# Performance work log

Hardware: AMD Instinct MI355X
Metric: run time of the kernel (lower is better)

## Reference

```python
import jax, jax.numpy as jnp
import numpy as np

NIN, NOUT = 256, 64

def setup_inputs() -> dict:
    key = jax.random.key(0)
    k1, k2, k3, k4 = jax.random.split(key, 4)
    B, T = 4, 4096
    y = jax.random.normal(k1, (B, T, NIN), dtype=jnp.float32)
    # torch Linear(nin, nout).weight has shape [nout, nin]; store as [nin, nout]
    s = 1.0 / np.sqrt(NIN)
    Wq = jax.random.uniform(k2, (NIN, NOUT), jnp.float32, -s, s)
    Wk = jax.random.uniform(k3, (NIN, NOUT), jnp.float32, -s, s)
    Wv = jax.random.uniform(k4, (NIN, NOUT), jnp.float32, -s, s)
    return {"y": y, "Wq": Wq, "Wk": Wk, "Wv": Wv}

def reference(y, Wq, Wk, Wv):
    T = y.shape[1]
    que = y @ Wq  # [B,T,NOUT]
    key = y @ Wk
    val = y @ Wv
    att = jnp.einsum('bqd,bkd->bqk', que, key)  # [B,T,T]
    causal = jnp.tril(jnp.ones((T, T), dtype=bool))  # True = keep
    att = jnp.where(causal, att, -jnp.inf)
    att = jax.nn.softmax(att / jnp.sqrt(jnp.float32(NOUT)), axis=-1)
    return jnp.einsum('bqk,bkd->bqd', att, val)
```

## Files before the change

### kernel.cpp

```cpp
#include <hip/hip_runtime.h>
#include <hip/hip_bf16.h>

#define TLEN 4096
#define NINP 256
#define DD   64

#define QSCALE 0.18033688011112042f

typedef __attribute__((ext_vector_type(8))) short bf16x8;
typedef __attribute__((ext_vector_type(4))) float f32x4;

union U8 { bf16x8 v; uint u[4]; };
union F32U { float f; uint u; };

__device__ inline ushort bfu(float x) {
    F32U a; a.f = x;
    uint r = a.u + 0x7fffu + ((a.u >> 16) & 1u);
    return (ushort)(r >> 16);
}
__device__ inline uint pk2(float p0, float p1) {
    F32U a, b; a.f = p0; b.f = p1;
    return __builtin_amdgcn_perm(b.u + 0x8000u, a.u + 0x8000u, 0x07060302u);
}
__device__ inline bf16x8 ld16(const ushort* p) {
    return *(const bf16x8*)p;
}
__device__ inline bf16x8 ld8x2(const ushort* p) {
    U8 u;
    uint2 a = *(const uint2*)p;
    uint2 b = *(const uint2*)(p + 4);
    u.u[0] = a.x; u.u[1] = a.y; u.u[2] = b.x; u.u[3] = b.y;
    return u.v;
}

__global__ __launch_bounds__(256) void prep_wt(
    const float* __restrict__ Wq, const float* __restrict__ Wk,
    const float* __restrict__ Wv, ushort* __restrict__ WT)
{
    const int t = threadIdx.x;
    const int m = blockIdx.x >> 4;
    const int d0 = (blockIdx.x & 15) * 4;
    const float* W = (m == 0) ? Wq : ((m == 1) ? Wk : Wv);
    const float scale = (m == 0) ? QSCALE : 1.0f;
    float4 v = *(const float4*)&W[t * DD + d0];
    WT[m * 16384 + (d0 + 0) * 256 + t] = bfu(v.x * scale);
    WT[m * 16384 + (d0 + 1) * 256 + t] = bfu(v.y * scale);
    WT[m * 16384 + (d0 + 2) * 256 + t] = bfu(v.z * scale);
    WT[m * 16384 + (d0 + 3) * 256 + t] = bfu(v.w * scale);
}

__global__ __launch_bounds__(256, 2) void qkv_kernel(
    const float* __restrict__ y, const ushort* __restrict__ WT,
    ushort* __restrict__ Qh, ushort* __restrict__ Kh, ushort* __restrict__ VhT)
{
    __shared__ ushort Wl[64 * 260];
    __shared__ ushort tb[2304];

    const int t = threadIdx.x;
    const int w = t >> 6, lane = t & 63;
    const int quad = lane >> 4, l15 = lane & 15;
    const int rgrp = w & 1, ngrp = w >> 1;
    const int rowbase = blockIdx.x * 32;
    const int myrow = rowbase + rgrp * 16 + l15;

    bf16x8 afrag[8];
    const float* yrow = y + (size_t)myrow * NINP;
    #pragma unroll
    for (int s = 0; s < 8; ++s) {
        float4 lo = *(const float4*)&yrow[s * 32 + quad * 8];
        float4 hi = *(const float4*)&yrow[s * 32 + quad * 8 + 4];
        U8 u;
        u.u[0] = bfu(lo.x) | (uint(bfu(lo.y)) << 16);
        u.u[1] = bfu(lo.z) | (uint(bfu(lo.w)) << 16);
        u.u[2] = bfu(hi.x) | (uint(bfu(hi.y)) << 16);
        u.u[3] = bfu(hi.z) | (uint(bfu(hi.w)) << 16);
        afrag[s] = u.v;
    }

    f32x4 acc[3][2];
    #pragma unroll
    for (int m = 0; m < 3; ++m)
        #pragma unroll
        for (int nj = 0; nj < 2; ++nj)
            acc[m][nj] = f32x4{0.f, 0.f, 0.f, 0.f};

    for (int m = 0; m < 3; ++m) {
        __syncthreads();
        {
            int n = t >> 2, seg = t & 3;
            const ushort* src = WT + m * 16384 + n * 256 + seg * 64;
            ushort* dst = &Wl[n * 260 + seg * 64];
            #pragma unroll
            for (int j = 0; j < 16; ++j)
                ((uint2*)dst)[j] = ((const uint2*)src)[j];
        }
        __syncthreads();
        #pragma unroll
        for (int s = 0; s < 8; ++s)
            #pragma unroll
            for (int nj = 0; nj < 2; ++nj) {
                int nt = ngrp * 2 + nj;
                bf16x8 bfrag = ld8x2(&Wl[(nt * 16 + l15) * 260 + s * 32 + quad * 8]);
                acc[m][nj] = __builtin_amdgcn_mfma_f32_16x16x32_bf16(
                    afrag[s], bfrag, acc[m][nj], 0, 0, 0);
            }
    }

    for (int m = 0; m < 2; ++m) {
        __syncthreads();
        #pragma unroll
        for (int nj = 0; nj < 2; ++nj) {
            int nt = ngrp * 2 + nj;
            #pragma unroll
            for (int r = 0; r < 4; ++r)
                tb[(rgrp * 16 + quad * 4 + r) * 68 + nt * 16 + l15] = bfu(acc[m][nj][r]);
        }
        __syncthreads();
        int row = t >> 3, c0 = (t & 7) * 8;
        ushort* gd = (m == 0 ? Qh : Kh) + (size_t)(rowbase + row) * DD + c0;
        const ushort* sp = &tb[row * 68 + c0];
        ((uint2*)gd)[0] = ((const uint2*)sp)[0];
        ((uint2*)gd)[1] = ((const uint2*)sp)[1];
    }

    __syncthreads();
    #pragma unroll
    for (int nj = 0; nj < 2; ++nj) {
        int nt = ngrp * 2 + nj;
        int d = nt * 16 + l15;
        #pragma unroll
        for (int r = 0; r < 4; r += 2) {
            int tt = rgrp * 16 + quad * 4 + r;
            *(uint*)&tb[d * 36 + tt] = pk2(acc[2][nj][r], acc[2][nj][r + 1]);
        }
    }
    __syncthreads();
    {
        int d = t >> 2, seg = t & 3;
        int bb = blockIdx.x >> 7;
        int tofs = (blockIdx.x & 127) * 32 + seg * 8;
        ushort* gv = VhT + ((size_t)bb * DD + d) * TLEN + tofs;
        const ushort* sp = &tb[d * 36 + seg * 8];
        ((uint2*)gv)[0] = ((const uint2*)sp)[0];
        ((uint2*)gv)[1] = ((const uint2*)sp)[1];
    }
}

template <bool MASK>
__device__ inline void softmax_store(
    f32x4 st[2][4], ushort* Pw, int qb, int c0, int l15, int quad, float* l_acc)
{
    #pragma unroll
    for (int qt = 0; qt < 2; ++qt) {
        const int q = qb + qt * 16 + l15;
        #pragma unroll
        for (int kt = 0; kt < 4; ++kt) {
            const int kbase = c0 + kt * 16 + quad * 4;
            float p[4];
            #pragma unroll
            for (int r = 0; r < 4; ++r) {
                float e = exp2f(st[qt][kt][r]);
                p[r] = (!MASK || (kbase + r <= q)) ? e : 0.f;
                l_acc[qt] += p[r];
            }
            ushort* pw = Pw + (qt * 16 + l15) * 68 + kt * 16 + quad * 4;
            *(uint*)&pw[0] = pk2(p[0], p[1]);
            *(uint*)&pw[2] = pk2(p[2], p[3]);
        }
    }
}

__global__ __launch_bounds__(512, 2) void attn_kernel(
    const ushort* __restrict__ Qh, const ushort* __restrict__ Kh,
    const ushort* __restrict__ VhT, float* __restrict__ out)
{
    __shared__ ushort Pb[8][32 * 68];
    __shared__ float  Ob[8][2048];
    __shared__ float  lb[8][32];

    const int t = threadIdx.x;
    const int w = t >> 6, lane = t & 63;
    const int quad = lane >> 4, l15 = lane & 15;
    const int b = blockIdx.x >> 6;
    const int pr = blockIdx.x & 63;

    const ushort* Qb = Qh + (size_t)b * TLEN * DD;
    const ushort* Kb = Kh + (size_t)b * TLEN * DD;
    const ushort* Vb = VhT + (size_t)b * DD * TLEN;
    float* outb = out + (size_t)b * TLEN * DD;

    for (int half = 0; half < 2; ++half) {
        const int tile = (half == 0) ? pr : (127 - pr);
        const int seg  = (half == 0) ? w : (7 - w);
        const int qb   = tile * 32;
        const int nc   = (tile + 2) >> 1;
        const int cps  = (nc + 7) >> 3;
        const int clo  = seg * cps;
        const int chi  = (nc < clo + cps) ? nc : (clo + cps);

        f32x4 o_acc[2][4];
        #pragma unroll
        for (int qt = 0; qt < 2; ++qt)
            #pragma unroll
            for (int nt = 0; nt < 4; ++nt)
                o_acc[qt][nt] = f32x4{0.f, 0.f, 0.f, 0.f};
        float l_acc[2] = {0.f, 0.f};

        if (clo < chi) {
            bf16x8 qf[2][2];
            #pragma unroll
            for (int qt = 0; qt < 2; ++qt)
                #pragma unroll
                for (int s = 0; s < 2; ++s)
                    qf[qt][s] = ld16(Qb + (size_t)(qb + qt * 16 + l15) * DD + s * 32 + quad * 8);

            bf16x8 kf[4][2];
            {
                int c0 = clo * 64;
                #pragma unroll
                for (int kt = 0; kt < 4; ++kt)
                    #pragma unroll
                    for (int s = 0; s < 2; ++s)
                        kf[kt][s] = ld16(Kb + (size_t)(c0 + kt * 16 + l15) * DD + s * 32 + quad * 8);
            }

            for (int ci = clo; ci < chi; ++ci) {
                const int c0 = ci * 64;
                bf16x8 vf[4][2];
                #pragma unroll
                for (int nt = 0; nt < 4; ++nt)
                    #pragma unroll
                    for (int s = 0; s < 2; ++s)
                        vf[nt][s] = ld16(Vb + (size_t)(nt * 16 + l15) * TLEN + c0 + s * 32 + quad * 8);

                f32x4 st[2][4];
                #pragma unroll
                for (int qt = 0; qt < 2; ++qt)
                    #pragma unroll
                    for (int kt = 0; kt < 4; ++kt)
                        st[qt][kt] = f32x4{0.f, 0.f, 0.f, 0.f};
                #pragma unroll
                for (int s = 0; s < 2; ++s)
                    #pragma unroll
                    for (int qt = 0; qt < 2; ++qt)
                        #pragma unroll
                        for (int kt = 0; kt < 4; ++kt)
                            st[qt][kt] = __builtin_amdgcn_mfma_f32_16x16x32_bf16(
                                kf[kt][s], qf[qt][s], st[qt][kt], 0, 0, 0);

                if (ci + 1 < chi) {
                    int c1 = c0 + 64;
                    #pragma unroll
                    for (int kt = 0; kt < 4; ++kt)
                        #pragma unroll
                        for (int s = 0; s < 2; ++s)
                            kf[kt][s] = ld16(Kb + (size_t)(c1 + kt * 16 + l15) * DD + s * 32 + quad * 8);
                }

                if (ci == nc - 1)
                    softmax_store<true>(st, Pb[w], qb, c0, l15, quad, l_acc);
                else
                    softmax_store<false>(st, Pb[w], qb, c0, l15, quad, l_acc);

                #pragma unroll
                for (int qt = 0; qt < 2; ++qt) {
                    const ushort* pr_ = &Pb[w][(qt * 16 + l15) * 68];
                    bf16x8 ap0 = ld8x2(pr_ + quad * 8);
                    bf16x8 ap1 = ld8x2(pr_ + 32 + quad * 8);
                    #pragma unroll
                    for (int nt = 0; nt < 4; ++nt) {
                        o_acc[qt][nt] = __builtin_amdgcn_mfma_f32_16x16x32_bf16(
                            ap0, vf[nt][0], o_acc[qt][nt], 0, 0, 0);
                        o_acc[qt][nt] = __builtin_amdgcn_mfma_f32_16x16x32_bf16(
                            ap1, vf[nt][1], o_acc[qt][nt], 0, 0, 0);
                    }
                }
            }

            #pragma unroll
            for (int qt = 0; qt < 2; ++qt) {
                l_acc[qt] += __shfl_xor(l_acc[qt], 16, 64);
                l_acc[qt] += __shfl_xor(l_acc[qt], 32, 64);
            }
        }

        #pragma unroll
        for (int qt = 0; qt < 2; ++qt) {
            #pragma unroll
            for (int nt = 0; nt < 4; ++nt)
                #pragma unroll
                for (int r = 0; r < 4; ++r)
                    Ob[w][(qt * 16 + quad * 4 + r) * 64 + nt * 16 + l15] = o_acc[qt][nt][r];
            if (quad == 0) lb[w][qt * 16 + l15] = l_acc[qt];
        }
        __syncthreads();

        {
            int q = t >> 4, d0 = (t & 15) * 4;
            f32x4 s = f32x4{0.f, 0.f, 0.f, 0.f};
            float ls = 0.f;
            #pragma unroll
            for (int ww = 0; ww < 8; ++ww) {
                s += *(const f32x4*)&Ob[ww][q * 64 + d0];
                ls += lb[ww][q];
            }
            float inv = __builtin_amdgcn_rcpf(ls);
            float4 r;
            r.x = s[0] * inv; r.y = s[1] * inv; r.z = s[2] * inv; r.w = s[3] * inv;
            *(float4*)&outb[(size_t)(qb + q) * DD + d0] = r;
        }
        __syncthreads();
    }
}

extern "C" void kernel_launch(void* const* d_in, const int* in_sizes, int n_in,
                              void* d_out, int out_size, void* d_ws, size_t ws_size,
                              hipStream_t stream) {
    const float* y  = (const float*)d_in[0];
    const float* Wq = (const float*)d_in[1];
    const float* Wk = (const float*)d_in[2];
    const float* Wv = (const float*)d_in[3];
    float* outp = (float*)d_out;

    const int rows = in_sizes[0] / NINP;
    const int nb = rows / TLEN;

    ushort* WT  = (ushort*)d_ws;
    ushort* Qh  = WT + 3 * 16384;
    ushort* Kh  = Qh + (size_t)rows * DD;
    ushort* VhT = Kh + (size_t)rows * DD;

    prep_wt<<<48, 256, 0, stream>>>(Wq, Wk, Wv, WT);
    qkv_kernel<<<rows / 32, 256, 0, stream>>>(y, WT, Qh, Kh, VhT);
    attn_kernel<<<nb * 64, 512, 0, stream>>>(Qh, Kh, VhT, outp);
}
```

Baseline: 116.5 us.

## Fuse QKV projection and attention into one kernel with per-batch grid barrier

Merges the QKV projection and attention kernels into a single launch. Each block first projects 64 rows, then waits on a per-batch atomic counter before running attention. Blocks drop from 512 to 256 threads, so the key-chunk split per tile goes from 8 waves to 4, and shared memory is reused through a union. This removes one kernel launch and the gap between kernels, but it relies on all 256 blocks being co-resident for the spin barrier and halves the waves available for attention parallelism.

```diff
diff --git a/kernel.cpp b/kernel.cpp
--- a/kernel.cpp
+++ b/kernel.cpp
@@ -35,8 +35,9 @@
 
 __global__ __launch_bounds__(256) void prep_wt(
     const float* __restrict__ Wq, const float* __restrict__ Wk,
-    const float* __restrict__ Wv, ushort* __restrict__ WT)
+    const float* __restrict__ Wv, ushort* __restrict__ WT, uint* __restrict__ cnt)
 {
+    if (blockIdx.x == 0 && threadIdx.x < 8) cnt[threadIdx.x] = 0;
     const int t = threadIdx.x;
     const int m = blockIdx.x >> 4;
     const int d0 = (blockIdx.x & 15) * 4;
@@ -49,102 +50,10 @@
     WT[m * 16384 + (d0 + 3) * 256 + t] = bfu(v.w * scale);
 }
 
-__global__ __launch_bounds__(256, 2) void qkv_kernel(
-    const float* __restrict__ y, const ushort* __restrict__ WT,
-    ushort* __restrict__ Qh, ushort* __restrict__ Kh, ushort* __restrict__ VhT)
-{
-    __shared__ ushort Wl[64 * 260];
-    __shared__ ushort tb[2304];
-
-    const int t = threadIdx.x;
-    const int w = t >> 6, lane = t & 63;
-    const int quad = lane >> 4, l15 = lane & 15;
-    const int rgrp = w & 1, ngrp = w >> 1;
-    const int rowbase = blockIdx.x * 32;
-    const int myrow = rowbase + rgrp * 16 + l15;
-
-    bf16x8 afrag[8];
-    const float* yrow = y + (size_t)myrow * NINP;
-    #pragma unroll
-    for (int s = 0; s < 8; ++s) {
-        float4 lo = *(const float4*)&yrow[s * 32 + quad * 8];
-        float4 hi = *(const float4*)&yrow[s * 32 + quad * 8 + 4];
-        U8 u;
-        u.u[0] = bfu(lo.x) | (uint(bfu(lo.y)) << 16);
-        u.u[1] = bfu(lo.z) | (uint(bfu(lo.w)) << 16);
-        u.u[2] = bfu(hi.x) | (uint(bfu(hi.y)) << 16);
-        u.u[3] = bfu(hi.z) | (uint(bfu(hi.w)) << 16);
-        afrag[s] = u.v;
-    }
-
-    f32x4 acc[3][2];
-    #pragma unroll
-    for (int m = 0; m < 3; ++m)
-        #pragma unroll
-        for (int nj = 0; nj < 2; ++nj)
-            acc[m][nj] = f32x4{0.f, 0.f, 0.f, 0.f};
-
-    for (int m = 0; m < 3; ++m) {
-        __syncthreads();
-        {
-            int n = t >> 2, seg = t & 3;
-            const ushort* src = WT + m * 16384 + n * 256 + seg * 64;
-            ushort* dst = &Wl[n * 260 + seg * 64];
-            #pragma unroll
-            for (int j = 0; j < 16; ++j)
-                ((uint2*)dst)[j] = ((const uint2*)src)[j];
-        }
-        __syncthreads();
-        #pragma unroll
-        for (int s = 0; s < 8; ++s)
-            #pragma unroll
-            for (int nj = 0; nj < 2; ++nj) {
-                int nt = ngrp * 2 + nj;
-                bf16x8 bfrag = ld8x2(&Wl[(nt * 16 + l15) * 260 + s * 32 + quad * 8]);
-                acc[m][nj] = __builtin_amdgcn_mfma_f32_16x16x32_bf16(
-                    afrag[s], bfrag, acc[m][nj], 0, 0, 0);
-            }
-    }
-
-    for (int m = 0; m < 2; ++m) {
-        __syncthreads();
-        #pragma unroll
-        for (int nj = 0; nj < 2; ++nj) {
-            int nt = ngrp * 2 + nj;
-            #pragma unroll
-            for (int r = 0; r < 4; ++r)
-                tb[(rgrp * 16 + quad * 4 + r) * 68 + nt * 16 + l15] = bfu(acc[m][nj][r]);
-        }
-        __syncthreads();
-        int row = t >> 3, c0 = (t & 7) * 8;
-        ushort* gd = (m == 0 ? Qh : Kh) + (size_t)(rowbase + row) * DD + c0;
-        const ushort* sp = &tb[row * 68 + c0];
-        ((uint2*)gd)[0] = ((const uint2*)sp)[0];
-        ((uint2*)gd)[1] = ((const uint2*)sp)[1];
-    }
-
-    __syncthreads();
-    #pragma unroll
-    for (int nj = 0; nj < 2; ++nj) {
-        int nt = ngrp * 2 + nj;
-        int d = nt * 16 + l15;
-        #pragma unroll
-        for (int r = 0; r < 4; r += 2) {
-            int tt = rgrp * 16 + quad * 4 + r;
-            *(uint*)&tb[d * 36 + tt] = pk2(acc[2][nj][r], acc[2][nj][r + 1]);
-        }
-    }
-    __syncthreads();
-    {
-        int d = t >> 2, seg = t & 3;
-        int bb = blockIdx.x >> 7;
-        int tofs = (blockIdx.x & 127) * 32 + seg * 8;
-        ushort* gv = VhT + ((size_t)bb * DD + d) * TLEN + tofs;
-        const ushort* sp = &tb[d * 36 + seg * 8];
-        ((uint2*)gv)[0] = ((const uint2*)sp)[0];
-        ((uint2*)gv)[1] = ((const uint2*)sp)[1];
-    }
-}
+union SMem {
+    struct { ushort Wl[64 * 260]; ushort tb[64 * 68]; } a;
+    struct { ushort Pb[4][32 * 68]; float Ob[4][2048]; float lb[4][32]; } b;
+};
 
 template <bool MASK>
 __device__ inline void softmax_store(
@@ -170,19 +79,110 @@
     }
 }
 
-__global__ __launch_bounds__(512, 2) void attn_kernel(
-    const ushort* __restrict__ Qh, const ushort* __restrict__ Kh,
-    const ushort* __restrict__ VhT, float* __restrict__ out)
+__global__ __launch_bounds__(256, 1) void fused_kernel(
+    const float* __restrict__ y, const ushort* __restrict__ WT,
+    ushort* __restrict__ Qh, ushort* __restrict__ Kh, ushort* __restrict__ VhT,
+    float* __restrict__ out, uint* __restrict__ cnt)
 {
-    __shared__ ushort Pb[8][32 * 68];
-    __shared__ float  Ob[8][2048];
-    __shared__ float  lb[8][32];
-
+    __shared__ SMem sm;
     const int t = threadIdx.x;
     const int w = t >> 6, lane = t & 63;
     const int quad = lane >> 4, l15 = lane & 15;
-    const int b = blockIdx.x >> 6;
-    const int pr = blockIdx.x & 63;
+    const int blk = blockIdx.x;
+    const int b = blk >> 6, pr = blk & 63;
+
+    {
+        const int rowbase = blk * 64;
+        const int myrow = rowbase + w * 16 + l15;
+
+        bf16x8 afrag[8];
+        const float* yrow = y + (size_t)myrow * NINP;
+        #pragma unroll
+        for (int s = 0; s < 8; ++s) {
+            float4 lo = *(const float4*)&yrow[s * 32 + quad * 8];
+            float4 hi = *(const float4*)&yrow[s * 32 + quad * 8 + 4];
+            U8 u;
+            u.u[0] = bfu(lo.x) | (uint(bfu(lo.y)) << 16);
+            u.u[1] = bfu(lo.z) | (uint(bfu(lo.w)) << 16);
+            u.u[2] = bfu(hi.x) | (uint(bfu(hi.y)) << 16);
+            u.u[3] = bfu(hi.z) | (uint(bfu(hi.w)) << 16);
+            afrag[s] = u.v;
+        }
+
+        f32x4 acc[3][4];
+        #pragma unroll
+        for (int m = 0; m < 3; ++m)
+            #pragma unroll
+            for (int nt = 0; nt < 4; ++nt)
+                acc[m][nt] = f32x4{0.f, 0.f, 0.f, 0.f};
+
+        for (int m = 0; m < 3; ++m) {
+            __syncthreads();
+            {
+                int n = t >> 2, seg = t & 3;
+                const ushort* src = WT + m * 16384 + n * 256 + seg * 64;
+                ushort* dst = &sm.a.Wl[n * 260 + seg * 64];
+                #pragma unroll
+                for (int j = 0; j < 16; ++j)
+                    ((uint2*)dst)[j] = ((const uint2*)src)[j];
+            }
+            __syncthreads();
+            #pragma unroll
+            for (int s = 0; s < 8; ++s)
+                #pragma unroll
+                for (int nt = 0; nt < 4; ++nt) {
+                    bf16x8 bfrag = ld8x2(&sm.a.Wl[(nt * 16 + l15) * 260 + s * 32 + quad * 8]);
+                    acc[m][nt] = __builtin_amdgcn_mfma_f32_16x16x32_bf16(
+                        afrag[s], bfrag, acc[m][nt], 0, 0, 0);
+                }
+        }
+
+        for (int m = 0; m < 2; ++m) {
+            __syncthreads();
+            #pragma unroll
+            for (int nt = 0; nt < 4; ++nt)
+                #pragma unroll
+                for (int r = 0; r < 4; ++r)
+                    sm.a.tb[(w * 16 + quad * 4 + r) * 68 + nt * 16 + l15] = bfu(acc[m][nt][r]);
+            __syncthreads();
+            int row = t >> 2, seg = t & 3;
+            ushort* gd = (m == 0 ? Qh : Kh) + (size_t)(rowbase + row) * DD + seg * 16;
+            const ushort* sp = &sm.a.tb[row * 68 + seg * 16];
+            #pragma unroll
+            for (int j = 0; j < 4; ++j) ((uint2*)gd)[j] = ((const uint2*)sp)[j];
+        }
+
+        __syncthreads();
+        #pragma unroll
+        for (int nt = 0; nt < 4; ++nt) {
+            int d = nt * 16 + l15;
+            #pragma unroll
+            for (int r = 0; r < 4; r += 2) {
+                int tt = w * 16 + quad * 4 + r;
+                *(uint*)&sm.a.tb[d * 68 + tt] = pk2(acc[2][nt][r], acc[2][nt][r + 1]);
+            }
+        }
+        __syncthreads();
+        {
+            int d = t >> 2, seg = t & 3;
+            int trow = pr * 64 + seg * 16;
+            ushort* gv = VhT + ((size_t)b * DD + d) * TLEN + trow;
+            const ushort* sp = &sm.a.tb[d * 68 + seg * 16];
+            #pragma unroll
+            for (int j = 0; j < 4; ++j) ((uint2*)gv)[j] = ((const uint2*)sp)[j];
+        }
+    }
+
+    __threadfence();
+    __syncthreads();
+    if (t == 0) {
+        __hip_atomic_fetch_add(&cnt[b], 1u, __ATOMIC_RELEASE, __HIP_MEMORY_SCOPE_AGENT);
+        while (__hip_atomic_load(&cnt[b], __ATOMIC_ACQUIRE, __HIP_MEMORY_SCOPE_AGENT) < 64u)
+            __builtin_amdgcn_s_sleep(8);
+    }
+    __syncthreads();
+    (void)__hip_atomic_load(&cnt[b], __ATOMIC_ACQUIRE, __HIP_MEMORY_SCOPE_AGENT);
+    __threadfence();
 
     const ushort* Qb = Qh + (size_t)b * TLEN * DD;
     const ushort* Kb = Kh + (size_t)b * TLEN * DD;
@@ -191,10 +191,10 @@
 
     for (int half = 0; half < 2; ++half) {
         const int tile = (half == 0) ? pr : (127 - pr);
-        const int seg  = (half == 0) ? w : (7 - w);
+        const int seg  = (half == 0) ? w : (3 - w);
         const int qb   = tile * 32;
         const int nc   = (tile + 2) >> 1;
-        const int cps  = (nc + 7) >> 3;
+        const int cps  = (nc + 3) >> 2;
         const int clo  = seg * cps;
         const int chi  = (nc < clo + cps) ? nc : (clo + cps);
 
@@ -258,13 +258,13 @@
                 }
 
                 if (ci == nc - 1)
-                    softmax_store<true>(st, Pb[w], qb, c0, l15, quad, l_acc);
+                    softmax_store<true>(st, sm.b.Pb[w], qb, c0, l15, quad, l_acc);
                 else
-                    softmax_store<false>(st, Pb[w], qb, c0, l15, quad, l_acc);
+                    softmax_store<false>(st, sm.b.Pb[w], qb, c0, l15, quad, l_acc);
 
                 #pragma unroll
                 for (int qt = 0; qt < 2; ++qt) {
-                    const ushort* pr_ = &Pb[w][(qt * 16 + l15) * 68];
+                    const ushort* pr_ = &sm.b.Pb[w][(qt * 16 + l15) * 68];
                     bf16x8 ap0 = ld8x2(pr_ + quad * 8);
                     bf16x8 ap1 = ld8x2(pr_ + 32 + quad * 8);
                     #pragma unroll
@@ -290,24 +290,28 @@
             for (int nt = 0; nt < 4; ++nt)
                 #pragma unroll
                 for (int r = 0; r < 4; ++r)
-                    Ob[w][(qt * 16 + quad * 4 + r) * 64 + nt * 16 + l15] = o_acc[qt][nt][r];
-            if (quad == 0) lb[w][qt * 16 + l15] = l_acc[qt];
+                    sm.b.Ob[w][(qt * 16 + quad * 4 + r) * 64 + nt * 16 + l15] = o_acc[qt][nt][r];
+            if (quad == 0) sm.b.lb[w][qt * 16 + l15] = l_acc[qt];
         }
         __syncthreads();
 
         {
-            int q = t >> 4, d0 = (t & 15) * 4;
-            f32x4 s = f32x4{0.f, 0.f, 0.f, 0.f};
+            int q = t >> 3, d0 = (t & 7) * 8;
+            f32x4 s0 = f32x4{0.f, 0.f, 0.f, 0.f};
+            f32x4 s1 = f32x4{0.f, 0.f, 0.f, 0.f};
             float ls = 0.f;
             #pragma unroll
-            for (int ww = 0; ww < 8; ++ww) {
-                s += *(const f32x4*)&Ob[ww][q * 64 + d0];
-                ls += lb[ww][q];
+            for (int ww = 0; ww < 4; ++ww) {
+                s0 += *(const f32x4*)&sm.b.Ob[ww][q * 64 + d0];
+                s1 += *(const f32x4*)&sm.b.Ob[ww][q * 64 + d0 + 4];
+                ls += sm.b.lb[ww][q];
             }
             float inv = __builtin_amdgcn_rcpf(ls);
-            float4 r;
-            r.x = s[0] * inv; r.y = s[1] * inv; r.z = s[2] * inv; r.w = s[3] * inv;
-            *(float4*)&outb[(size_t)(qb + q) * DD + d0] = r;
+            float4 r0, r1;
+            r0.x = s0[0] * inv; r0.y = s0[1] * inv; r0.z = s0[2] * inv; r0.w = s0[3] * inv;
+            r1.x = s1[0] * inv; r1.y = s1[1] * inv; r1.z = s1[2] * inv; r1.w = s1[3] * inv;
+            *(float4*)&outb[(size_t)(qb + q) * DD + d0] = r0;
+            *(float4*)&outb[(size_t)(qb + q) * DD + d0 + 4] = r1;
         }
         __syncthreads();
     }
@@ -329,8 +333,8 @@
     ushort* Qh  = WT + 3 * 16384;
     ushort* Kh  = Qh + (size_t)rows * DD;
     ushort* VhT = Kh + (size_t)rows * DD;
-
-    prep_wt<<<48, 256, 0, stream>>>(Wq, Wk, Wv, WT);
-    qkv_kernel<<<rows / 32, 256, 0, stream>>>(y, WT, Qh, Kh, VhT);
-    attn_kernel<<<nb * 64, 512, 0, stream>>>(Qh, Kh, VhT, outp);
-}
+    uint*   cnt = (uint*)(VhT + (size_t)rows * DD);
+
+    prep_wt<<<48, 256, 0, stream>>>(Wq, Wk, Wv, WT, cnt);
+    fused_kernel<<<nb * 64, 256, 0, stream>>>(y, WT, Qh, Kh, VhT, outp, cnt);
+}
```

Result: slower. 183.2 us (+57.2%).

## Restructure attention: one 32-query tile per block with shared-memory K/V staging

Applied to the files above, without the earlier changes.

The attention kernel changes from 512-thread blocks, each handling a paired light/heavy tile split across 8 waves by KV chunks, to 256-thread blocks, each handling one 32-row query tile. K and V chunks are now loaded cooperatively into shared memory with register double-buffering, and the 4 waves split the work by query half and key half. Tiles are launched heaviest first to balance the load, and the final reduction only combines two partial results. This lowers per-wave global traffic and allows more resident blocks, but adds two barriers per chunk and drops the explicit light/heavy pairing.

```diff
diff --git a/kernel.cpp b/kernel.cpp
--- a/kernel.cpp
+++ b/kernel.cpp
@@ -146,170 +146,157 @@
     }
 }
 
-template <bool MASK>
-__device__ inline void softmax_store(
-    f32x4 st[2][4], ushort* Pw, int qb, int c0, int l15, int quad, float* l_acc)
-{
-    #pragma unroll
-    for (int qt = 0; qt < 2; ++qt) {
-        const int q = qb + qt * 16 + l15;
-        #pragma unroll
-        for (int kt = 0; kt < 4; ++kt) {
-            const int kbase = c0 + kt * 16 + quad * 4;
-            float p[4];
-            #pragma unroll
-            for (int r = 0; r < 4; ++r) {
-                float e = exp2f(st[qt][kt][r]);
-                p[r] = (!MASK || (kbase + r <= q)) ? e : 0.f;
-                l_acc[qt] += p[r];
-            }
-            ushort* pw = Pw + (qt * 16 + l15) * 68 + kt * 16 + quad * 4;
-            *(uint*)&pw[0] = pk2(p[0], p[1]);
-            *(uint*)&pw[2] = pk2(p[2], p[3]);
-        }
-    }
-}
-
-__global__ __launch_bounds__(512, 2) void attn_kernel(
+__global__ __launch_bounds__(256, 4) void attn_kernel(
     const ushort* __restrict__ Qh, const ushort* __restrict__ Kh,
     const ushort* __restrict__ VhT, float* __restrict__ out)
 {
-    __shared__ ushort Pb[8][32 * 68];
-    __shared__ float  Ob[8][2048];
-    __shared__ float  lb[8][32];
+    __shared__ ushort Kl[64 * 72];
+    __shared__ ushort Vt[64 * 72];
+    __shared__ ushort Pw[4][16 * 36];
+    __shared__ float  Ob[2][16 * 64];
+    __shared__ float  lb[2][2][16];
 
     const int t = threadIdx.x;
     const int w = t >> 6, lane = t & 63;
     const int quad = lane >> 4, l15 = lane & 15;
-    const int b = blockIdx.x >> 6;
-    const int pr = blockIdx.x & 63;
-
-    const ushort* Qb = Qh + (size_t)b * TLEN * DD;
-    const ushort* Kb = Kh + (size_t)b * TLEN * DD;
-    const ushort* Vb = VhT + (size_t)b * DD * TLEN;
-    float* outb = out + (size_t)b * TLEN * DD;
-
-    for (int half = 0; half < 2; ++half) {
-        const int tile = (half == 0) ? pr : (127 - pr);
-        const int seg  = (half == 0) ? w : (7 - w);
-        const int qb   = tile * 32;
-        const int nc   = (tile + 2) >> 1;
-        const int cps  = (nc + 7) >> 3;
-        const int clo  = seg * cps;
-        const int chi  = (nc < clo + cps) ? nc : (clo + cps);
-
-        f32x4 o_acc[2][4];
-        #pragma unroll
-        for (int qt = 0; qt < 2; ++qt)
-            #pragma unroll
-            for (int nt = 0; nt < 4; ++nt)
-                o_acc[qt][nt] = f32x4{0.f, 0.f, 0.f, 0.f};
-        float l_acc[2] = {0.f, 0.f};
-
-        if (clo < chi) {
-            bf16x8 qf[2][2];
-            #pragma unroll
-            for (int qt = 0; qt < 2; ++qt)
+    const int qt = w >> 1, g = w & 1;
+    const int blk = blockIdx.x;
+    const int batch = blk & 3;
+    const int tile = 127 - (blk >> 2);
+    const int qb = tile * 32;
+    const int nc = (tile + 2) >> 1;
+
+    const ushort* Qb = Qh + (size_t)batch * TLEN * DD;
+    const ushort* Kb = Kh + (size_t)batch * TLEN * DD;
+    const ushort* Vb = VhT + (size_t)batch * DD * TLEN;
+    float* outb = out + (size_t)batch * TLEN * DD;
+
+    bf16x8 qf[2];
+    #pragma unroll
+    for (int s = 0; s < 2; ++s)
+        qf[s] = ld16(Qb + (size_t)(qb + qt * 16 + l15) * DD + s * 32 + quad * 8);
+
+    const int srow = t >> 3, sseg = t & 7;
+
+    f32x4 o_acc[4];
+    #pragma unroll
+    for (int nt = 0; nt < 4; ++nt) o_acc[nt] = f32x4{0.f, 0.f, 0.f, 0.f};
+    float l_acc = 0.f;
+
+    uint4 ka, kb4, va, vb4;
+    {
+        const ushort* kp = Kb + (size_t)srow * DD + sseg * 8;
+        ka  = *(const uint4*)kp;
+        kb4 = *(const uint4*)(kp + 32 * DD);
+        const ushort* vp = Vb + (size_t)srow * TLEN + sseg * 8;
+        va  = *(const uint4*)vp;
+        vb4 = *(const uint4*)(vp + 32 * TLEN);
+    }
+
+    for (int ci = 0; ci < nc; ++ci) {
+        const int c0 = ci * 64;
+        __syncthreads();
+        *(uint4*)&Kl[srow * 72 + sseg * 8]        = ka;
+        *(uint4*)&Kl[(srow + 32) * 72 + sseg * 8] = kb4;
+        *(uint4*)&Vt[srow * 72 + sseg * 8]        = va;
+        *(uint4*)&Vt[(srow + 32) * 72 + sseg * 8] = vb4;
+        __syncthreads();
+
+        if (ci + 1 < nc) {
+            const int c1 = c0 + 64;
+            const ushort* kp = Kb + (size_t)(c1 + srow) * DD + sseg * 8;
+            ka  = *(const uint4*)kp;
+            kb4 = *(const uint4*)(kp + 32 * DD);
+            const ushort* vp = Vb + (size_t)srow * TLEN + c1 + sseg * 8;
+            va  = *(const uint4*)vp;
+            vb4 = *(const uint4*)(vp + 32 * TLEN);
+        }
+
+        bf16x8 kf[2][2];
+        #pragma unroll
+        for (int kt2 = 0; kt2 < 2; ++kt2)
+            #pragma unroll
+            for (int s = 0; s < 2; ++s)
+                kf[kt2][s] = ld16(&Kl[(g * 32 + kt2 * 16 + l15) * 72 + s * 32 + quad * 8]);
+
+        f32x4 st[2];
+        st[0] = f32x4{0.f, 0.f, 0.f, 0.f};
+        st[1] = f32x4{0.f, 0.f, 0.f, 0.f};
+        #pragma unroll
+        for (int s = 0; s < 2; ++s)
+            #pragma unroll
+            for (int kt2 = 0; kt2 < 2; ++kt2)
+                st[kt2] = __builtin_amdgcn_mfma_f32_16x16x32_bf16(
+                    kf[kt2][s], qf[s], st[kt2], 0, 0, 0);
+
+        bf16x8 vf[4];
+        #pragma unroll
+        for (int nt = 0; nt < 4; ++nt)
+            vf[nt] = ld16(&Vt[(nt * 16 + l15) * 72 + g * 32 + quad * 8]);
+
+        ushort* pwb = &Pw[w][l15 * 36 + quad * 4];
+        if (ci == nc - 1) {
+            const int q = qb + qt * 16 + l15;
+            #pragma unroll
+            for (int kt2 = 0; kt2 < 2; ++kt2) {
+                const int kbase = c0 + g * 32 + kt2 * 16 + quad * 4;
+                float p[4];
                 #pragma unroll
-                for (int s = 0; s < 2; ++s)
-                    qf[qt][s] = ld16(Qb + (size_t)(qb + qt * 16 + l15) * DD + s * 32 + quad * 8);
-
-            bf16x8 kf[4][2];
-            {
-                int c0 = clo * 64;
+                for (int r = 0; r < 4; ++r) {
+                    float e = exp2f(st[kt2][r]);
+                    p[r] = (kbase + r <= q) ? e : 0.f;
+                    l_acc += p[r];
+                }
+                *(uint*)&pwb[kt2 * 16]     = pk2(p[0], p[1]);
+                *(uint*)&pwb[kt2 * 16 + 2] = pk2(p[2], p[3]);
+            }
+        } else {
+            #pragma unroll
+            for (int kt2 = 0; kt2 < 2; ++kt2) {
+                float p[4];
                 #pragma unroll
-                for (int kt = 0; kt < 4; ++kt)
-                    #pragma unroll
-                    for (int s = 0; s < 2; ++s)
-                        kf[kt][s] = ld16(Kb + (size_t)(c0 + kt * 16 + l15) * DD + s * 32 + quad * 8);
+                for (int r = 0; r < 4; ++r) {
+                    p[r] = exp2f(st[kt2][r]);
+                    l_acc += p[r];
+                }
+                *(uint*)&pwb[kt2 * 16]     = pk2(p[0], p[1]);
+                *(uint*)&pwb[kt2 * 16 + 2] = pk2(p[2], p[3]);
             }
-
-            for (int ci = clo; ci < chi; ++ci) {
-                const int c0 = ci * 64;
-                bf16x8 vf[4][2];
-                #pragma unroll
-                for (int nt = 0; nt < 4; ++nt)
-                    #pragma unroll
-                    for (int s = 0; s < 2; ++s)
-                        vf[nt][s] = ld16(Vb + (size_t)(nt * 16 + l15) * TLEN + c0 + s * 32 + quad * 8);
-
-                f32x4 st[2][4];
-                #pragma unroll
-                for (int qt = 0; qt < 2; ++qt)
-                    #pragma unroll
-                    for (int kt = 0; kt < 4; ++kt)
-                        st[qt][kt] = f32x4{0.f, 0.f, 0.f, 0.f};
-                #pragma unroll
-                for (int s = 0; s < 2; ++s)
-                    #pragma unroll
-                    for (int qt = 0; qt < 2; ++qt)
-                        #pragma unroll
-                        for (int kt = 0; kt < 4; ++kt)
-                            st[qt][kt] = __builtin_amdgcn_mfma_f32_16x16x32_bf16(
-                                kf[kt][s], qf[qt][s], st[qt][kt], 0, 0, 0);
-
-                if (ci + 1 < chi) {
-                    int c1 = c0 + 64;
-                    #pragma unroll
-                    for (int kt = 0; kt < 4; ++kt)
-                        #pragma unroll
-                        for (int s = 0; s < 2; ++s)
-                            kf[kt][s] = ld16(Kb + (size_t)(c1 + kt * 16 + l15) * DD + s * 32 + quad * 8);
-                }
-
-                if (ci == nc - 1)
-                    softmax_store<true>(st, Pb[w], qb, c0, l15, quad, l_acc);
-                else
-                    softmax_store<false>(st, Pb[w], qb, c0, l15, quad, l_acc);
-
-                #pragma unroll
-                for (int qt = 0; qt < 2; ++qt) {
-                    const ushort* pr_ = &Pb[w][(qt * 16 + l15) * 68];
-                    bf16x8 ap0 = ld8x2(pr_ + quad * 8);
-                    bf16x8 ap1 = ld8x2(pr_ + 32 + quad * 8);
-                    #pragma unroll
-                    for (int nt = 0; nt < 4; ++nt) {
-                        o_acc[qt][nt] = __builtin_amdgcn_mfma_f32_16x16x32_bf16(
-                            ap0, vf[nt][0], o_acc[qt][nt], 0, 0, 0);
-                        o_acc[qt][nt] = __builtin_amdgcn_mfma_f32_16x16x32_bf16(
-                            ap1, vf[nt][1], o_acc[qt][nt], 0, 0, 0);
-                    }
-                }
+        }
+
+        bf16x8 ap = ld8x2(&Pw[w][l15 * 36 + quad * 8]);
+        #pragma unroll
+        for (int nt = 0; nt < 4; ++nt)
+            o_acc[nt] = __builtin_amdgcn_mfma_f32_16x16x32_bf16(
+                ap, vf[nt], o_acc[nt], 0, 0, 0);
+    }
+
+    l_acc += __shfl_xor(l_acc, 16, 64);
+    l_acc += __shfl_xor(l_acc, 32, 64);
+    if (quad == 0) lb[g][qt][l15] = l_acc;
+
+    if (g == 1) {
+        #pragma unroll
+        for (int nt = 0; nt < 4; ++nt)
+            #pragma unroll
+            for (int r = 0; r < 4; ++r)
+                Ob[qt][(quad * 4 + r) * 64 + nt * 16 + l15] = o_acc[nt][r];
+    }
+    __syncthreads();
+    if (g == 0) {
+        float linv[4];
+        #pragma unroll
+        for (int r = 0; r < 4; ++r) {
+            int q16 = quad * 4 + r;
+            linv[r] = __builtin_amdgcn_rcpf(lb[0][qt][q16] + lb[1][qt][q16]);
+        }
+        #pragma unroll
+        for (int nt = 0; nt < 4; ++nt)
+            #pragma unroll
+            for (int r = 0; r < 4; ++r) {
+                float v = o_acc[nt][r] + Ob[qt][(quad * 4 + r) * 64 + nt * 16 + l15];
+                outb[(size_t)(qb + qt * 16 + quad * 4 + r) * DD + nt * 16 + l15] = v * linv[r];
             }
-
-            #pragma unroll
-            for (int qt = 0; qt < 2; ++qt) {
-                l_acc[qt] += __shfl_xor(l_acc[qt], 16, 64);
-                l_acc[qt] += __shfl_xor(l_acc[qt], 32, 64);
-            }
-        }
-
-        #pragma unroll
-        for (int qt = 0; qt < 2; ++qt) {
-            #pragma unroll
-            for (int nt = 0; nt < 4; ++nt)
-                #pragma unroll
-                for (int r = 0; r < 4; ++r)
-                    Ob[w][(qt * 16 + quad * 4 + r) * 64 + nt * 16 + l15] = o_acc[qt][nt][r];
-            if (quad == 0) lb[w][qt * 16 + l15] = l_acc[qt];
-        }
-        __syncthreads();
-
-        {
-            int q = t >> 4, d0 = (t & 15) * 4;
-            f32x4 s = f32x4{0.f, 0.f, 0.f, 0.f};
-            float ls = 0.f;
-            #pragma unroll
-            for (int ww = 0; ww < 8; ++ww) {
-                s += *(const f32x4*)&Ob[ww][q * 64 + d0];
-                ls += lb[ww][q];
-            }
-            float inv = __builtin_amdgcn_rcpf(ls);
-            float4 r;
-            r.x = s[0] * inv; r.y = s[1] * inv; r.z = s[2] * inv; r.w = s[3] * inv;
-            *(float4*)&outb[(size_t)(qb + q) * DD + d0] = r;
-        }
-        __syncthreads();
     }
 }
 
@@ -332,5 +319,5 @@
 
     prep_wt<<<48, 256, 0, stream>>>(Wq, Wk, Wv, WT);
     qkv_kernel<<<rows / 32, 256, 0, stream>>>(y, WT, Qh, Kh, VhT);
-    attn_kernel<<<nb * 64, 512, 0, stream>>>(Qh, Kh, VhT, outp);
-}
+    attn_kernel<<<nb * 128, 256, 0, stream>>>(Qh, Kh, VhT, outp);
+}
```

Measured after the change: 116.5 us. Within noise of the previous version (-0.0%).
